# Kernel tuning notes

Measured on AMD Instinct MI355X. Metric: run time of the kernel, lower is better.

The kernel has to match this reference:

```python
import jax, jax.numpy as jnp
import numpy as np

ALPHA = 0.2  # LeakyReLU negative slope


def setup_inputs() -> dict:
    key = jax.random.key(0)
    k1, k2, k3, k4 = jax.random.split(key, 4)
    B, N, in_dim, out_dim, n_heads = 4, 2048, 128, 32, 4
    H = jax.random.normal(k1, (B, N, in_dim), dtype=jnp.float32)
    adj = jax.random.randint(k2, (N, N), 0, 2).astype(jnp.float32)
    # xavier-uniform-like init for params
    limW = np.sqrt(6.0 / (in_dim + out_dim))
    W = jax.random.uniform(k3, (n_heads, in_dim, out_dim), minval=-limW, maxval=limW, dtype=jnp.float32)
    lima = np.sqrt(6.0 / (n_heads + 2 * out_dim))
    a = jax.random.uniform(k4, (n_heads, 2 * out_dim), minval=-lima, maxval=lima, dtype=jnp.float32)
    return {"H": H, "adj": adj, "W": W, "a": a}


def reference(H, adj, W, a):
    B, N, _ = H.shape
    n_heads, _, out_dim = W.shape
    # projected features: (B, H, N, F)
    Ht = jnp.einsum('bni,hio->bhno', H, W)
    # split attention vector: e_ij = leaky_relu(a_src . h_i + a_dst . h_j)
    a_src, a_dst = a[:, :out_dim], a[:, out_dim:]
    src = jnp.einsum('bhnf,hf->bhn', Ht, a_src)  # (B,H,N)
    dst = jnp.einsum('bhnf,hf->bhn', Ht, a_dst)  # (B,H,N)
    e = src[:, :, :, None] + dst[:, :, None, :]  # (B,H,N,N)
    e = jnp.where(e >= 0, e, ALPHA * e)          # leaky_relu
    mask = (adj + jnp.eye(N, dtype=adj.dtype)) != 0  # (N,N) bool, self-loops added
    e = jnp.where(mask[None, None], e, -jnp.inf)
    alpha = jax.nn.softmax(e, axis=-1)           # (B,H,N,N)
    H_new = jnp.einsum('bhnj,bhjf->bhnf', alpha, Ht)
    H_new = jnp.where(H_new > 0, H_new, jnp.expm1(H_new))  # ELU
    # concat heads: (B, N, n_heads*out_dim)
    H_new = jnp.transpose(H_new, (0, 2, 1, 3)).reshape(B, N, n_heads * out_dim)
    return H_new, alpha
```

## Files before the change

kernel.cpp:

```cpp
#include <hip/hip_runtime.h>
#include <hip/hip_bf16.h>
#include <math.h>


typedef float f32x4 __attribute__((ext_vector_type(4)));
typedef short bf16x8 __attribute__((ext_vector_type(8)));
typedef unsigned int u32;

#define LRELU 0.2f
#define LOG2E 1.44269504088896f
#define EXP2(x) __builtin_amdgcn_exp2f(x)

__device__ inline ushort f2b(float x) {
    unsigned int u = __float_as_uint(x);
    u += 0x7fffu + ((u >> 16) & 1u);
    return (ushort)(u >> 16);
}

__global__ __launch_bounds__(256) void k0_adjI(const float* __restrict__ adj,
                                               unsigned char* __restrict__ adjI) {
    int idx = blockIdx.x * 256 + threadIdx.x;
    int e0 = idx * 4;
    int row = e0 >> 11;
    int c0 = e0 & 2047;
    float4 v = *(const float4*)(adj + (size_t)e0);
    uchar4 o;
    o.x = (v.x != 0.f || c0     == row) ? 1 : 0;
    o.y = (v.y != 0.f || c0 + 1 == row) ? 1 : 0;
    o.z = (v.z != 0.f || c0 + 2 == row) ? 1 : 0;
    o.w = (v.w != 0.f || c0 + 3 == row) ? 1 : 0;
    *(uchar4*)(adjI + (size_t)e0) = o;
}

__global__ __launch_bounds__(256) void k1_ht(const float* __restrict__ H,
                                             const float* __restrict__ W,
                                             const float* __restrict__ a,
                                             __hip_bfloat16* __restrict__ HtT,
                                             float* __restrict__ src,
                                             float* __restrict__ dst) {
    __shared__ __align__(16) ushort Wbf[32 * 128];

    int t = threadIdx.x;
    int ntile = blockIdx.x;
    int bh    = blockIdx.y;
    int b = bh >> 2, h = bh & 3;
    int lane = t & 63, w = t >> 6;
    int l15 = lane & 15, l4 = lane >> 4;

    #pragma unroll
    for (int u = 0; u < 16; ++u) {
        int idx = u * 256 + t;
        int i = idx >> 5, f = idx & 31;
        Wbf[(f * 128 + i) ^ ((f & 7) << 3)] = f2b(W[h * 4096 + idx]);
    }
    __syncthreads();

    int n = ntile * 64 + w * 16 + l15;
    const float* hrow = H + ((size_t)(b * 2048) + n) * 128;

    f32x4 acc0 = {0.f, 0.f, 0.f, 0.f};
    f32x4 acc1 = {0.f, 0.f, 0.f, 0.f};
    #pragma unroll
    for (int kc = 0; kc < 4; ++kc) {
        int k0 = kc * 32 + l4 * 8;
        float4 h0 = *(const float4*)(hrow + k0);
        float4 h1 = *(const float4*)(hrow + k0 + 4);
        union { u32 u[4]; bf16x8 v; } bu;
        asm("v_cvt_pk_bf16_f32 %0, %1, %2" : "=v"(bu.u[0]) : "v"(h0.x), "v"(h0.y));
        asm("v_cvt_pk_bf16_f32 %0, %1, %2" : "=v"(bu.u[1]) : "v"(h0.z), "v"(h0.w));
        asm("v_cvt_pk_bf16_f32 %0, %1, %2" : "=v"(bu.u[2]) : "v"(h1.x), "v"(h1.y));
        asm("v_cvt_pk_bf16_f32 %0, %1, %2" : "=v"(bu.u[3]) : "v"(h1.z), "v"(h1.w));
        bf16x8 bfrag = bu.v;
        bf16x8 af0 = *(const bf16x8*)&Wbf[(l15 * 128 + kc * 32 + l4 * 8) ^ ((l15 & 7) << 3)];
        bf16x8 af1 = *(const bf16x8*)&Wbf[((16 + l15) * 128 + kc * 32 + l4 * 8) ^ (((16 + l15) & 7) << 3)];
        acc0 = __builtin_amdgcn_mfma_f32_16x16x32_bf16(af0, bfrag, acc0, 0, 0, 0);
        acc1 = __builtin_amdgcn_mfma_f32_16x16x32_bf16(af1, bfrag, acc1, 0, 0, 0);
    }

    float sv = 0.f, dvv = 0.f;
    ushort* ht = (ushort*)HtT;
    #pragma unroll
    for (int r = 0; r < 4; ++r) {
        int f0 = l4 * 4 + r;
        sv  += acc0[r] * a[h * 64 + f0]      + acc1[r] * a[h * 64 + 16 + f0];
        dvv += acc0[r] * a[h * 64 + 32 + f0] + acc1[r] * a[h * 64 + 48 + f0];
        ht[(size_t)(bh * 32 + f0) * 2048 + n]      = f2b(acc0[r]);
        ht[(size_t)(bh * 32 + 16 + f0) * 2048 + n] = f2b(acc1[r]);
    }
    sv  += __shfl_xor(sv, 16);  sv  += __shfl_xor(sv, 32);
    dvv += __shfl_xor(dvv, 16); dvv += __shfl_xor(dvv, 32);
    if (l4 == 0) { src[bh * 2048 + n] = sv; dst[bh * 2048 + n] = dvv; }
}

__global__ __launch_bounds__(256, 4) void k2_fused(const unsigned char* __restrict__ adjI,
                                                   const float* __restrict__ src,
                                                   const float* __restrict__ dst,
                                                   const __hip_bfloat16* __restrict__ HtT,
                                                   float* __restrict__ alpha,
                                                   float* __restrict__ outH) {
    __shared__ float dstS[2048];
    __shared__ float rowL[32], rowSrcS[32];
    __shared__ __align__(16) ushort As[32 * 128];

    int t = threadIdx.x;
    int mtile = blockIdx.x;
    int bh    = blockIdx.y;
    int lane = t & 63, w = t >> 6;
    int b = bh >> 2, h = bh & 3;
    int row0 = mtile * 32;

    const float4* dst4g = (const float4*)(dst + bh * 2048);
    #pragma unroll
    for (int u = 0; u < 2; ++u) {
        float4 v = dst4g[u * 256 + t];
        v.x *= LOG2E; v.y *= LOG2E; v.z *= LOG2E; v.w *= LOG2E;
        *(float4*)&dstS[(u * 256 + t) * 4] = v;
    }
    if (t < 32) rowSrcS[t] = src[bh * 2048 + row0 + t] * LOG2E;
    __syncthreads();

    for (int rr = 0; rr < 8; ++rr) {
        int r = w * 8 + rr;
        int gr = row0 + r;
        float sn = rowSrcS[r];
        const uint2* a8 = (const uint2*)(adjI + (size_t)gr * 2048);
        float S = 0.f;
        #pragma unroll
        for (int u = 0; u < 4; ++u) {
            uint2 ab = a8[u * 64 + lane];
            int jb = (u * 64 + lane) * 8;
            float4 dv0 = *(const float4*)&dstS[jb];
            float4 dv1 = *(const float4*)&dstS[jb + 4];
            float dj[8] = {dv0.x, dv0.y, dv0.z, dv0.w, dv1.x, dv1.y, dv1.z, dv1.w};
            #pragma unroll
            for (int q = 0; q < 8; ++q) {
                u32 word = (q < 4) ? ab.x : ab.y;
                float ajf = (float)((word >> (8 * (q & 3))) & 0xffu);
                float ee = sn + dj[q];
                float vm = fmaxf(ee, LRELU * ee);
                S = fmaf(EXP2(vm), ajf, S);
            }
        }
        #pragma unroll
        for (int off = 32; off; off >>= 1) S += __shfl_xor(S, off);
        if (lane == 0) rowL[r] = -__log2f(S);
    }
    __syncthreads();

    f32x4 acc = {0.f, 0.f, 0.f, 0.f};
    int wr = w >> 1, wc = w & 1;
    int l15 = lane & 15, l4 = lane >> 4;
    int arow = wr * 16 + l15;
    const ushort* Bfp = (const ushort*)HtT + (size_t)(bh * 32 + wc * 16 + l15) * 2048 + l4 * 8;
    float* alphaRow = alpha + (size_t)(bh * 2048 + row0) * 2048;

    int sr = t >> 5;
    int sc4 = t & 31;

    float snR[4], LR[4];
    #pragma unroll
    for (int u = 0; u < 4; ++u) { snR[u] = rowSrcS[sr + u * 8]; LR[u] = rowL[sr + u * 8]; }

    auto loadA = [&](int k, u32* ar) {
        #pragma unroll
        for (int u = 0; u < 4; ++u)
            ar[u] = *(const u32*)(adjI + (size_t)(row0 + sr + u * 8) * 2048 + k * 128 + sc4 * 4);
    };
    auto loadB = [&](int k, bf16x8* br) {
        #pragma unroll
        for (int kk = 0; kk < 4; ++kk)
            br[kk] = *(const bf16x8*)(Bfp + (size_t)k * 128 + kk * 32);
    };
    auto stage = [&](int k, const u32* ar) {
        int jb = k * 128 + sc4 * 4;
        float4 dv = *(const float4*)&dstS[jb];
        float dj[4] = {dv.x, dv.y, dv.z, dv.w};
        #pragma unroll
        for (int u = 0; u < 4; ++u) {
            int r = sr + u * 8;
            float sn = snR[u], L = LR[u];
            u32 ab = ar[u];
            float o[4];
            #pragma unroll
            for (int q = 0; q < 4; ++q) {
                float ajf = (float)((ab >> (8 * q)) & 0xffu);
                float ee = sn + dj[q];
                float vm = fmaxf(ee + L, fmaf(ee, LRELU, L));
                o[q] = EXP2(vm) * ajf;
            }
            f32x4 ov = {o[0], o[1], o[2], o[3]};
            __builtin_nontemporal_store(ov, (f32x4*)(alphaRow + (size_t)r * 2048 + jb));
            u32 lo, hi;
            asm("v_cvt_pk_bf16_f32 %0, %1, %2" : "=v"(lo) : "v"(o[0]), "v"(o[1]));
            asm("v_cvt_pk_bf16_f32 %0, %1, %2" : "=v"(hi) : "v"(o[2]), "v"(o[3]));
            uint2 pk = {lo, hi};
            *(uint2*)&As[(r * 128 + sc4 * 4) ^ ((r & 7) << 3)] = pk;
        }
    };
    auto mfmaPhase = [&](const bf16x8* br) {
        #pragma unroll
        for (int kk = 0; kk < 4; ++kk) {
            bf16x8 af = *(const bf16x8*)&As[(arow * 128 + kk * 32 + l4 * 8) ^ ((arow & 7) << 3)];
            acc = __builtin_amdgcn_mfma_f32_16x16x32_bf16(af, br[kk], acc, 0, 0, 0);
        }
    };

    u32 aE[4], aO[4];
    bf16x8 bE[4], bO[4];
    loadA(0, aE); loadB(0, bE);

    for (int kp = 0; kp < 8; ++kp) {
        int ke = 2 * kp, ko = 2 * kp + 1;
        if (ke) { asm volatile("s_waitcnt lgkmcnt(0)" ::: "memory"); __builtin_amdgcn_s_barrier(); }
        loadA(ko, aO); loadB(ko, bO);
        __builtin_amdgcn_sched_barrier(0);
        stage(ke, aE);
        asm volatile("s_waitcnt lgkmcnt(0)" ::: "memory");
        __builtin_amdgcn_s_barrier();
        mfmaPhase(bE);
        asm volatile("s_waitcnt lgkmcnt(0)" ::: "memory");
        __builtin_amdgcn_s_barrier();
        if (ko + 1 < 16) { loadA(ko + 1, aE); loadB(ko + 1, bE); }
        __builtin_amdgcn_sched_barrier(0);
        stage(ko, aO);
        asm volatile("s_waitcnt lgkmcnt(0)" ::: "memory");
        __builtin_amdgcn_s_barrier();
        mfmaPhase(bO);
    }

    #pragma unroll
    for (int q = 0; q < 4; ++q) {
        int node = row0 + wr * 16 + l4 * 4 + q;
        float v = acc[q];
        v = (v > 0.f) ? v : expm1f(v);
        outH[(size_t)(b * 2048 + node) * 128 + h * 32 + wc * 16 + l15] = v;
    }
}

extern "C" void kernel_launch(void* const* d_in, const int* in_sizes, int n_in,
                              void* d_out, int out_size, void* d_ws, size_t ws_size,
                              hipStream_t stream) {
    const float* H   = (const float*)d_in[0];
    const float* adj = (const float*)d_in[1];
    const float* W   = (const float*)d_in[2];
    const float* a   = (const float*)d_in[3];

    float* outH  = (float*)d_out;
    float* alpha = outH + (size_t)4 * 2048 * 128;

    char* ws = (char*)d_ws;
    __hip_bfloat16* HtT = (__hip_bfloat16*)ws;
    float* src = (float*)(ws + 2 * 1024 * 1024);
    float* dst = src + 32768;
    unsigned char* adjI = (unsigned char*)(ws + 2 * 1024 * 1024 + 256 * 1024);

    k0_adjI<<<4096, 256, 0, stream>>>(adj, adjI);
    k1_ht<<<dim3(32, 16), 256, 0, stream>>>(H, W, a, HtT, src, dst);
    k2_fused<<<dim3(64, 16), 256, 0, stream>>>(adjI, src, dst, HtT, alpha, outH);
}
```

Before: 75.56 us.

## Merge preprocessing kernels, coalesce HtT stores, double-buffer attention LDS tiles

```diff
diff --git a/kernel.cpp b/kernel.cpp
--- a/kernel.cpp
+++ b/kernel.cpp
@@ -17,32 +17,36 @@
     return (ushort)(u >> 16);
 }
 
-__global__ __launch_bounds__(256) void k0_adjI(const float* __restrict__ adj,
-                                               unsigned char* __restrict__ adjI) {
-    int idx = blockIdx.x * 256 + threadIdx.x;
-    int e0 = idx * 4;
-    int row = e0 >> 11;
-    int c0 = e0 & 2047;
-    float4 v = *(const float4*)(adj + (size_t)e0);
-    uchar4 o;
-    o.x = (v.x != 0.f || c0     == row) ? 1 : 0;
-    o.y = (v.y != 0.f || c0 + 1 == row) ? 1 : 0;
-    o.z = (v.z != 0.f || c0 + 2 == row) ? 1 : 0;
-    o.w = (v.w != 0.f || c0 + 3 == row) ? 1 : 0;
-    *(uchar4*)(adjI + (size_t)e0) = o;
-}
-
-__global__ __launch_bounds__(256) void k1_ht(const float* __restrict__ H,
-                                             const float* __restrict__ W,
-                                             const float* __restrict__ a,
-                                             __hip_bfloat16* __restrict__ HtT,
-                                             float* __restrict__ src,
-                                             float* __restrict__ dst) {
+__global__ __launch_bounds__(256) void k01(const float* __restrict__ adj,
+                                           unsigned char* __restrict__ adjI,
+                                           const float* __restrict__ H,
+                                           const float* __restrict__ W,
+                                           const float* __restrict__ a,
+                                           __hip_bfloat16* __restrict__ HtT,
+                                           float* __restrict__ src,
+                                           float* __restrict__ dst) {
     __shared__ __align__(16) ushort Wbf[32 * 128];
 
+    int bid = blockIdx.x;
     int t = threadIdx.x;
-    int ntile = blockIdx.x;
-    int bh    = blockIdx.y;
+
+    if (bid >= 512) {
+        int idx = (bid - 512) * 256 + t;
+        int e0 = idx * 4;
+        int row = e0 >> 11;
+        int c0 = e0 & 2047;
+        float4 v = *(const float4*)(adj + (size_t)e0);
+        uchar4 o;
+        o.x = (v.x != 0.f || c0     == row) ? 1 : 0;
+        o.y = (v.y != 0.f || c0 + 1 == row) ? 1 : 0;
+        o.z = (v.z != 0.f || c0 + 2 == row) ? 1 : 0;
+        o.w = (v.w != 0.f || c0 + 3 == row) ? 1 : 0;
+        *(uchar4*)(adjI + (size_t)e0) = o;
+        return;
+    }
+
+    int ntile = bid & 31;
+    int bh = bid >> 5;
     int b = bh >> 2, h = bh & 3;
     int lane = t & 63, w = t >> 6;
     int l15 = lane & 15, l4 = lane >> 4;
@@ -78,21 +82,34 @@
     }
 
     float sv = 0.f, dvv = 0.f;
-    ushort* ht = (ushort*)HtT;
     #pragma unroll
     for (int r = 0; r < 4; ++r) {
         int f0 = l4 * 4 + r;
         sv  += acc0[r] * a[h * 64 + f0]      + acc1[r] * a[h * 64 + 16 + f0];
         dvv += acc0[r] * a[h * 64 + 32 + f0] + acc1[r] * a[h * 64 + 48 + f0];
-        ht[(size_t)(bh * 32 + f0) * 2048 + n]      = f2b(acc0[r]);
-        ht[(size_t)(bh * 32 + 16 + f0) * 2048 + n] = f2b(acc1[r]);
     }
     sv  += __shfl_xor(sv, 16);  sv  += __shfl_xor(sv, 32);
     dvv += __shfl_xor(dvv, 16); dvv += __shfl_xor(dvv, 32);
     if (l4 == 0) { src[bh * 2048 + n] = sv; dst[bh * 2048 + n] = dvv; }
-}
-
-__global__ __launch_bounds__(256, 4) void k2_fused(const unsigned char* __restrict__ adjI,
+
+    __syncthreads();
+    ushort* T = Wbf;
+    int nl = w * 16 + l15;
+    #pragma unroll
+    for (int r = 0; r < 4; ++r) {
+        int f0 = l4 * 4 + r;
+        T[f0 * 64 + nl]        = f2b(acc0[r]);
+        T[(16 + f0) * 64 + nl] = f2b(acc1[r]);
+    }
+    __syncthreads();
+    {
+        int f = t >> 3, n8 = (t & 7) * 8;
+        uint4 v = *(const uint4*)&T[f * 64 + n8];
+        *(uint4*)((ushort*)HtT + (size_t)(bh * 32 + f) * 2048 + ntile * 64 + n8) = v;
+    }
+}
+
+__global__ __launch_bounds__(256, 6) void k2_fused(const unsigned char* __restrict__ adjI,
                                                    const float* __restrict__ src,
                                                    const float* __restrict__ dst,
                                                    const __hip_bfloat16* __restrict__ HtT,
@@ -100,7 +117,7 @@
                                                    float* __restrict__ outH) {
     __shared__ float dstS[2048];
     __shared__ float rowL[32], rowSrcS[32];
-    __shared__ __align__(16) ushort As[32 * 128];
+    __shared__ __align__(16) ushort As[2][32 * 128];
 
     int t = threadIdx.x;
     int mtile = blockIdx.x;
@@ -123,22 +140,24 @@
         int r = w * 8 + rr;
         int gr = row0 + r;
         float sn = rowSrcS[r];
-        const uint2* a8 = (const uint2*)(adjI + (size_t)gr * 2048);
+        const uint4* a16 = (const uint4*)(adjI + (size_t)gr * 2048);
         float S = 0.f;
         #pragma unroll
-        for (int u = 0; u < 4; ++u) {
-            uint2 ab = a8[u * 64 + lane];
-            int jb = (u * 64 + lane) * 8;
-            float4 dv0 = *(const float4*)&dstS[jb];
-            float4 dv1 = *(const float4*)&dstS[jb + 4];
-            float dj[8] = {dv0.x, dv0.y, dv0.z, dv0.w, dv1.x, dv1.y, dv1.z, dv1.w};
+        for (int u = 0; u < 2; ++u) {
+            uint4 ab = a16[u * 64 + lane];
+            int jb = (u * 64 + lane) * 16;
+            u32 words[4] = {ab.x, ab.y, ab.z, ab.w};
             #pragma unroll
-            for (int q = 0; q < 8; ++q) {
-                u32 word = (q < 4) ? ab.x : ab.y;
-                float ajf = (float)((word >> (8 * (q & 3))) & 0xffu);
-                float ee = sn + dj[q];
-                float vm = fmaxf(ee, LRELU * ee);
-                S = fmaf(EXP2(vm), ajf, S);
+            for (int wq = 0; wq < 4; ++wq) {
+                float4 dv = *(const float4*)&dstS[jb + wq * 4];
+                float dj[4] = {dv.x, dv.y, dv.z, dv.w};
+                #pragma unroll
+                for (int q = 0; q < 4; ++q) {
+                    float ajf = (float)((words[wq] >> (8 * q)) & 0xffu);
+                    float ee = sn + dj[q];
+                    float vm = fmaxf(ee, LRELU * ee);
+                    S = fmaf(EXP2(vm), ajf, S);
+                }
             }
         }
         #pragma unroll
@@ -171,7 +190,7 @@
         for (int kk = 0; kk < 4; ++kk)
             br[kk] = *(const bf16x8*)(Bfp + (size_t)k * 128 + kk * 32);
     };
-    auto stage = [&](int k, const u32* ar) {
+    auto stage = [&](int k, const u32* ar, ushort* Asb) {
         int jb = k * 128 + sc4 * 4;
         float4 dv = *(const float4*)&dstS[jb];
         float dj[4] = {dv.x, dv.y, dv.z, dv.w};
@@ -194,13 +213,13 @@
             asm("v_cvt_pk_bf16_f32 %0, %1, %2" : "=v"(lo) : "v"(o[0]), "v"(o[1]));
             asm("v_cvt_pk_bf16_f32 %0, %1, %2" : "=v"(hi) : "v"(o[2]), "v"(o[3]));
             uint2 pk = {lo, hi};
-            *(uint2*)&As[(r * 128 + sc4 * 4) ^ ((r & 7) << 3)] = pk;
+            *(uint2*)&Asb[(r * 128 + sc4 * 4) ^ ((r & 7) << 3)] = pk;
         }
     };
-    auto mfmaPhase = [&](const bf16x8* br) {
+    auto mfmaPhase = [&](const bf16x8* br, const ushort* Asb) {
         #pragma unroll
         for (int kk = 0; kk < 4; ++kk) {
-            bf16x8 af = *(const bf16x8*)&As[(arow * 128 + kk * 32 + l4 * 8) ^ ((arow & 7) << 3)];
+            bf16x8 af = *(const bf16x8*)&Asb[(arow * 128 + kk * 32 + l4 * 8) ^ ((arow & 7) << 3)];
             acc = __builtin_amdgcn_mfma_f32_16x16x32_bf16(af, br[kk], acc, 0, 0, 0);
         }
     };
@@ -211,21 +230,18 @@
 
     for (int kp = 0; kp < 8; ++kp) {
         int ke = 2 * kp, ko = 2 * kp + 1;
-        if (ke) { asm volatile("s_waitcnt lgkmcnt(0)" ::: "memory"); __builtin_amdgcn_s_barrier(); }
         loadA(ko, aO); loadB(ko, bO);
         __builtin_amdgcn_sched_barrier(0);
-        stage(ke, aE);
+        stage(ke, aE, As[0]);
         asm volatile("s_waitcnt lgkmcnt(0)" ::: "memory");
         __builtin_amdgcn_s_barrier();
-        mfmaPhase(bE);
+        mfmaPhase(bE, As[0]);
+        if (ko + 1 < 16) { loadA(ko + 1, aE); loadB(ko + 1, bE); }
+        __builtin_amdgcn_sched_barrier(0);
+        stage(ko, aO, As[1]);
         asm volatile("s_waitcnt lgkmcnt(0)" ::: "memory");
         __builtin_amdgcn_s_barrier();
-        if (ko + 1 < 16) { loadA(ko + 1, aE); loadB(ko + 1, bE); }
-        __builtin_amdgcn_sched_barrier(0);
-        stage(ko, aO);
-        asm volatile("s_waitcnt lgkmcnt(0)" ::: "memory");
-        __builtin_amdgcn_s_barrier();
-        mfmaPhase(bO);
+        mfmaPhase(bO, As[1]);
     }
 
     #pragma unroll
@@ -254,7 +270,6 @@
     float* dst = src + 32768;
     unsigned char* adjI = (unsigned char*)(ws + 2 * 1024 * 1024 + 256 * 1024);
 
-    k0_adjI<<<4096, 256, 0, stream>>>(adj, adjI);
-    k1_ht<<<dim3(32, 16), 256, 0, stream>>>(H, W, a, HtT, src, dst);
+    k01<<<4608, 256, 0, stream>>>(adj, adjI, H, W, a, HtT, src, dst);
     k2_fused<<<dim3(64, 16), 256, 0, stream>>>(adjI, src, dst, HtT, alpha, outH);
 }
```

Measured after the change: 108.6 us. +43.7%, slower.
